# Kernel tuning notes

Measured on AMD Instinct MI355X. Metric: run time of the kernel, lower is better.

The kernel has to match this reference:

```python
import jax, jax.numpy as jnp
import numpy as np

N_NODES = 100000


def gcn_conv(x, edge_index, W, b):
    """PyG-style GCNConv: symmetric-normalized A+I propagation of x @ W, plus bias."""
    n = x.shape[0]
    src, dst = edge_index[0], edge_index[1]
    loops = jnp.arange(n, dtype=src.dtype)
    src = jnp.concatenate([src, loops])  # add self loops
    dst = jnp.concatenate([dst, loops])
    deg = jax.ops.segment_sum(jnp.ones_like(src, dtype=x.dtype), dst, num_segments=n)
    dinv = jnp.where(deg > 0, jax.lax.rsqrt(deg), 0.0)
    norm = dinv[src] * dinv[dst]  # [E+n]
    h = x @ W  # [n, out]
    msg = h[src] * norm[:, None]  # gather + scale
    out = jax.ops.segment_sum(msg, dst, num_segments=n)  # scatter-add
    return out + b


def setup_inputs() -> dict:
    key = jax.random.key(0)
    ks = jax.random.split(key, 5)
    x = jax.random.normal(ks[0], (N_NODES, 4), dtype=jnp.float32)
    edge_index = jax.random.randint(ks[1], (2, 3200000), 0, N_NODES, dtype=jnp.int64)
    W1 = jax.random.normal(ks[2], (4, 64), dtype=jnp.float32) * 0.5
    b1 = jnp.zeros((64,), dtype=jnp.float32)
    W2 = jax.random.normal(ks[3], (64, 32), dtype=jnp.float32) * 0.125
    b2 = jnp.zeros((32,), dtype=jnp.float32)
    return {"x": x, "edge_index": edge_index, "W1": W1, "b1": b1, "W2": W2, "b2": b2}


def reference(x, edge_index, W1, b1, W2, b2):
    h = gcn_conv(x, edge_index, W1, b1)
    h = jax.nn.relu(h)
    # F.dropout with training=False is identity (eval-mode reference)
    h = gcn_conv(h, edge_index, W2, b2)
    return jnp.mean(h, axis=0)  # [32]
```

## Files before the change

### kernel.cpp

```cpp
#include <hip/hip_runtime.h>

#define ST 512
#define EPB 8192
#define HT 1024
#define FT 1024
#define S_LOG 8
#define S 256
#define CAP 8912
#define MAXB 512
#define FXS 8388608.0f
#define FXI 1.1920929e-7f

__device__ __forceinline__ void gAtomAdd(float* p, float v) {
    unsafeAtomicAdd(p, v);
}

__global__ void k_init(int* __restrict__ cur_d, int* __restrict__ cur_s,
                       float* __restrict__ g, int nb) {
    int t = threadIdx.x;
    if (t < nb) { cur_d[t] = t * CAP; cur_s[t] = t * CAP; }
    if (t < 64) g[t] = 0.0f;
}

__global__ void __launch_bounds__(ST) k_sctr2(
        const int4* __restrict__ src4, const int4* __restrict__ dst4, int E,
        int* __restrict__ cur_d, int* __restrict__ cur_s,
        unsigned* __restrict__ rec_d, unsigned* __restrict__ rec_s, int nb) {
    __shared__ unsigned lrec[EPB];
    __shared__ unsigned short lbkt[EPB];
    __shared__ int cnt[MAXB];
    __shared__ int lst[MAXB];
    __shared__ int gb[MAXB];
    __shared__ int wsum[8];
    int t = threadIdx.x;
    int lane = t & 63, wv = t >> 6;
    int E4 = E >> 2;
    int b4 = blockIdx.x * (EPB / 4);
    int m = min(EPB, E - blockIdx.x * EPB);

    int4 dk[4], sk[4];
    bool v[4];
    #pragma unroll
    for (int k = 0; k < 4; ++k) {
        int idx = b4 + k * ST + t;
        v[k] = idx < E4;
        if (v[k]) { dk[k] = dst4[idx]; sk[k] = src4[idx]; }
    }

    for (int ph = 0; ph < 2; ++ph) {
        int* cursor = ph ? cur_s : cur_d;
        unsigned* rec = ph ? rec_s : rec_d;
        cnt[t] = 0;
        __syncthreads();
        int rk[16];
        #pragma unroll
        for (int k = 0; k < 4; ++k) {
            if (v[k]) {
                int4 K = ph ? sk[k] : dk[k];
                rk[4 * k + 0] = atomicAdd(&cnt[K.x >> S_LOG], 1);
                rk[4 * k + 1] = atomicAdd(&cnt[K.y >> S_LOG], 1);
                rk[4 * k + 2] = atomicAdd(&cnt[K.z >> S_LOG], 1);
                rk[4 * k + 3] = atomicAdd(&cnt[K.w >> S_LOG], 1);
            }
        }
        __syncthreads();
        int c = cnt[t];
        int ic = c;
        #pragma unroll
        for (int o = 1; o < 64; o <<= 1) {
            int u = __shfl_up(ic, o);
            if (lane >= o) ic += u;
        }
        if (lane == 63) wsum[wv] = ic;
        __syncthreads();
        int pre = 0;
        #pragma unroll
        for (int k = 0; k < 7; ++k) pre += (k < wv) ? wsum[k] : 0;
        ic += pre;
        lst[t] = ic - c;
        gb[t] = (c > 0) ? atomicAdd(&cursor[t], c) : 0;
        __syncthreads();
        #pragma unroll
        for (int k = 0; k < 4; ++k) {
            if (v[k]) {
                int4 K = ph ? sk[k] : dk[k];
                int4 P = ph ? dk[k] : sk[k];
                int bb, p;
                bb = K.x >> S_LOG; p = lst[bb] + rk[4 * k + 0];
                lrec[p] = ((unsigned)P.x << S_LOG) | (unsigned)(K.x & (S - 1));
                lbkt[p] = (unsigned short)bb;
                bb = K.y >> S_LOG; p = lst[bb] + rk[4 * k + 1];
                lrec[p] = ((unsigned)P.y << S_LOG) | (unsigned)(K.y & (S - 1));
                lbkt[p] = (unsigned short)bb;
                bb = K.z >> S_LOG; p = lst[bb] + rk[4 * k + 2];
                lrec[p] = ((unsigned)P.z << S_LOG) | (unsigned)(K.z & (S - 1));
                lbkt[p] = (unsigned short)bb;
                bb = K.w >> S_LOG; p = lst[bb] + rk[4 * k + 3];
                lrec[p] = ((unsigned)P.w << S_LOG) | (unsigned)(K.w & (S - 1));
                lbkt[p] = (unsigned short)bb;
            }
        }
        __syncthreads();
        for (int i = t; i < m; i += ST) {
            int bb = lbkt[i];
            rec[gb[bb] + (i - lst[bb])] = lrec[i];
        }
        __syncthreads();
    }
}

__global__ void __launch_bounds__(HT) k_hist(
        const unsigned* __restrict__ rec_d, const int* __restrict__ cur_d,
        const float4* __restrict__ x, float* __restrict__ dinv,
        float4* __restrict__ y, int n) {
    __shared__ int cnt[S];
    int b = blockIdx.x, t = threadIdx.x;
    if (t < S) cnt[t] = 0;
    __syncthreads();
    int lo = b * CAP;
    int m = cur_d[b] - lo;
    int m4 = m >> 2;
    const uint4* rec4 = (const uint4*)(rec_d + lo);
    for (int i = t; i < m4; i += HT) {
        uint4 r = rec4[i];
        atomicAdd(&cnt[r.x & (S - 1)], 1);
        atomicAdd(&cnt[r.y & (S - 1)], 1);
        atomicAdd(&cnt[r.z & (S - 1)], 1);
        atomicAdd(&cnt[r.w & (S - 1)], 1);
    }
    for (int i = (m4 << 2) + t; i < m; i += HT)
        atomicAdd(&cnt[rec_d[lo + i] & (S - 1)], 1);
    __syncthreads();
    int nd = (b << S_LOG) + t;
    if (t < S && nd < n) {
        float dv = rsqrtf((float)cnt[t] + 1.0f);
        dinv[nd] = dv;
        float4 xi = x[nd];
        y[nd] = make_float4(dv * xi.x, dv * xi.y, dv * xi.z, dv * xi.w);
    }
}

__global__ void __launch_bounds__(FT) k_fuse(
        const unsigned* __restrict__ rec_d, const unsigned* __restrict__ rec_s,
        const int* __restrict__ cur_d, const int* __restrict__ cur_s,
        const float4* __restrict__ y, const float* __restrict__ dinv,
        const float* __restrict__ W1, const float* __restrict__ b1,
        float* __restrict__ g, int n) {
    __shared__ unsigned lrec[CAP];
    __shared__ int cnt[S];
    __shared__ int nst[S];
    __shared__ int ia[S];
    __shared__ float4 lp1[S];
    __shared__ float red[FT];
    __shared__ int wsum[4];
    int b = blockIdx.x, t = threadIdx.x;
    int lane = t & 63, wv = t >> 6;
    if (t < S) { cnt[t] = 0; ia[t] = 0; }
    __syncthreads();
    int lo = b * CAP;
    int md = cur_d[b] - lo;
    unsigned rv[9]; int rr[9];
    #pragma unroll
    for (int k = 0; k < 9; ++k) {
        int i = t + k * FT;
        if (i < md) {
            unsigned r = rec_d[lo + i];
            rv[k] = r;
            rr[k] = atomicAdd(&cnt[r & (S - 1)], 1);
        }
    }
    __syncthreads();
    int c = 0, ic = 0;
    if (t < S) {
        c = cnt[t]; ic = c;
        #pragma unroll
        for (int o = 1; o < 64; o <<= 1) {
            int u = __shfl_up(ic, o);
            if (lane >= o) ic += u;
        }
        if (lane == 63) wsum[wv] = ic;
    }
    __syncthreads();
    if (t < S) {
        int pre = 0;
        #pragma unroll
        for (int k = 0; k < 3; ++k) pre += (k < wv) ? wsum[k] : 0;
        ic += pre;
        cnt[t] = ic;
        nst[t] = ic - c;
    }
    __syncthreads();
    #pragma unroll
    for (int k = 0; k < 9; ++k) {
        int i = t + k * FT;
        if (i < md) lrec[nst[rv[k] & (S - 1)] + rr[k]] = rv[k] >> S_LOG;
    }
    int ms = cur_s[b] - lo;
    int ms4 = ms >> 2;
    const uint4* rs4 = (const uint4*)(rec_s + lo);
    for (int i = t; i < ms4; i += FT) {
        uint4 r = rs4[i];
        int d0 = (int)(dinv[r.x >> S_LOG] * FXS + 0.5f);
        int d1 = (int)(dinv[r.y >> S_LOG] * FXS + 0.5f);
        int d2 = (int)(dinv[r.z >> S_LOG] * FXS + 0.5f);
        int d3 = (int)(dinv[r.w >> S_LOG] * FXS + 0.5f);
        atomicAdd(&ia[r.x & (S - 1)], d0);
        atomicAdd(&ia[r.y & (S - 1)], d1);
        atomicAdd(&ia[r.z & (S - 1)], d2);
        atomicAdd(&ia[r.w & (S - 1)], d3);
    }
    for (int i = (ms4 << 2) + t; i < ms; i += FT) {
        unsigned r = rec_s[lo + i];
        atomicAdd(&ia[r & (S - 1)], (int)(dinv[r >> S_LOG] * FXS + 0.5f));
    }
    __syncthreads();
    int node = t >> 2, q = t & 3;
    int nd = (b << S_LOG) + node;
    if (nd < n) {
        int j1 = cnt[node];
        int j = nst[node] + q;
        float a0 = 0.0f, a1 = 0.0f, a2 = 0.0f, a3 = 0.0f;
        for (; j + 12 < j1; j += 16) {
            int s0 = lrec[j], s1 = lrec[j + 4], s2 = lrec[j + 8], s3 = lrec[j + 12];
            float4 y0 = y[s0], y1 = y[s1], y2 = y[s2], y3 = y[s3];
            a0 += y0.x + y1.x + y2.x + y3.x;
            a1 += y0.y + y1.y + y2.y + y3.y;
            a2 += y0.z + y1.z + y2.z + y3.z;
            a3 += y0.w + y1.w + y2.w + y3.w;
        }
        for (; j < j1; j += 4) {
            float4 ys = y[lrec[j]];
            a0 += ys.x; a1 += ys.y; a2 += ys.z; a3 += ys.w;
        }
        a0 += __shfl_down(a0, 2); a1 += __shfl_down(a1, 2);
        a2 += __shfl_down(a2, 2); a3 += __shfl_down(a3, 2);
        a0 += __shfl_down(a0, 1); a1 += __shfl_down(a1, 1);
        a2 += __shfl_down(a2, 1); a3 += __shfl_down(a3, 1);
        if (q == 0) {
            float di = dinv[nd];
            lp1[node] = make_float4(di * a0, di * a1, di * a2, di * a3);
        }
    }
    __syncthreads();
    int cch = t & 63, w = t >> 6;
    float w0 = W1[cch], w1 = W1[64 + cch], w2 = W1[128 + cch], w3 = W1[192 + cch];
    float bb = b1[cch];
    int nb0 = b << S_LOG;
    float facc = 0.0f;
    for (int k = w; k < S; k += 16) {
        int ndk = nb0 + k;
        if (ndk >= n) break;
        float di = dinv[ndk];
        float4 p = lp1[k];
        float4 yi = y[ndk];
        float h0 = fmaf(di, yi.x, p.x);
        float h1 = fmaf(di, yi.y, p.y);
        float h2 = fmaf(di, yi.z, p.z);
        float h3 = fmaf(di, yi.w, p.w);
        float h = fmaf(h0, w0, fmaf(h1, w1, fmaf(h2, w2, fmaf(h3, w3, bb))));
        h = fmaxf(h, 0.0f);
        float ak = (float)ia[k] * FXI;
        float wi = fmaf(di, ak, di * di);
        facc = fmaf(wi, h, facc);
    }
    red[t] = facc;
    __syncthreads();
    if (t < 64) {
        float s = red[t];
        #pragma unroll
        for (int o = 1; o < 16; ++o) s += red[t + 64 * o];
        gAtomAdd(&g[t], s);
    }
}

__global__ void k_final(const float* __restrict__ g, const float* __restrict__ W2,
                        const float* __restrict__ b2, float* __restrict__ out, float inv_n) {
    int j = threadIdx.x;
    if (j < 32) {
        float a = 0.0f;
        #pragma unroll
        for (int c = 0; c < 64; ++c) a = fmaf(g[c], W2[c * 32 + j], a);
        out[j] = fmaf(a, inv_n, b2[j]);
    }
}

extern "C" void kernel_launch(void* const* d_in, const int* in_sizes, int n_in,
                              void* d_out, int out_size, void* d_ws, size_t ws_size,
                              hipStream_t stream) {
    const float* x  = (const float*)d_in[0];
    const int*   ei = (const int*)d_in[1];
    const float* W1 = (const float*)d_in[2];
    const float* b1 = (const float*)d_in[3];
    const float* W2 = (const float*)d_in[4];
    const float* b2 = (const float*)d_in[5];
    float* out = (float*)d_out;

    int n = in_sizes[0] / 4;
    int E = in_sizes[1] / 2;
    const int* src = ei;
    const int* dst = ei + E;
    int NB = (n + S - 1) >> S_LOG;

    char* ws = (char*)d_ws;
    int* cur_d = (int*)ws;
    int* cur_s = cur_d + 512;
    float* g   = (float*)(cur_s + 512);
    size_t ctrl = 1600;
    unsigned* rec_d = (unsigned*)ws + ctrl;
    unsigned* rec_s = rec_d + (size_t)NB * CAP;
    float* y    = (float*)(rec_s + (size_t)NB * CAP);
    float* dinv = y + 4 * (size_t)n;

    int NSB = (E + EPB - 1) / EPB;

    k_init<<<1, 512, 0, stream>>>(cur_d, cur_s, g, NB);
    k_sctr2<<<NSB, ST, 0, stream>>>((const int4*)src, (const int4*)dst, E,
                                    cur_d, cur_s, rec_d, rec_s, NB);
    k_hist<<<NB, HT, 0, stream>>>(rec_d, cur_d, (const float4*)x, dinv,
                                  (float4*)y, n);
    k_fuse<<<NB, FT, 0, stream>>>(rec_d, rec_s, cur_d, cur_s,
                                  (const float4*)y, dinv, W1, b1, g, n);
    k_final<<<1, 64, 0, stream>>>(g, W2, b2, out, 1.0f / (float)n);
}
```

Measured before the change: 146.0 us.

## Fold final projection into fuse kernel, replace init kernel with memset, widen scatter blocks

The separate k_final launch is removed. The last block of k_fuse, found through an atomic ticket counter, now does the 64x32 projection. The init kernel becomes a hipMemsetAsync, with cursors changed to zero-based offsets. The scatter kernel now uses 1024 threads per block with 2 int4 loads per thread instead of 512 threads with 4. Together this cuts launch overhead at the cost of a threadfence/ticket pattern in k_fuse.

```diff
diff --git a/kernel.cpp b/kernel.cpp
--- a/kernel.cpp
+++ b/kernel.cpp
@@ -1,6 +1,6 @@
 #include <hip/hip_runtime.h>
 
-#define ST 512
+#define ST 1024
 #define EPB 8192
 #define HT 1024
 #define FT 1024
@@ -13,13 +13,6 @@
 
 __device__ __forceinline__ void gAtomAdd(float* p, float v) {
     unsafeAtomicAdd(p, v);
-}
-
-__global__ void k_init(int* __restrict__ cur_d, int* __restrict__ cur_s,
-                       float* __restrict__ g, int nb) {
-    int t = threadIdx.x;
-    if (t < nb) { cur_d[t] = t * CAP; cur_s[t] = t * CAP; }
-    if (t < 64) g[t] = 0.0f;
 }
 
 __global__ void __launch_bounds__(ST) k_sctr2(
@@ -38,10 +31,10 @@
     int b4 = blockIdx.x * (EPB / 4);
     int m = min(EPB, E - blockIdx.x * EPB);
 
-    int4 dk[4], sk[4];
-    bool v[4];
+    int4 dk[2], sk[2];
+    bool v[2];
     #pragma unroll
-    for (int k = 0; k < 4; ++k) {
+    for (int k = 0; k < 2; ++k) {
         int idx = b4 + k * ST + t;
         v[k] = idx < E4;
         if (v[k]) { dk[k] = dst4[idx]; sk[k] = src4[idx]; }
@@ -50,11 +43,11 @@
     for (int ph = 0; ph < 2; ++ph) {
         int* cursor = ph ? cur_s : cur_d;
         unsigned* rec = ph ? rec_s : rec_d;
-        cnt[t] = 0;
-        __syncthreads();
-        int rk[16];
-        #pragma unroll
-        for (int k = 0; k < 4; ++k) {
+        if (t < MAXB) cnt[t] = 0;
+        __syncthreads();
+        int rk[8];
+        #pragma unroll
+        for (int k = 0; k < 2; ++k) {
             if (v[k]) {
                 int4 K = ph ? sk[k] : dk[k];
                 rk[4 * k + 0] = atomicAdd(&cnt[K.x >> S_LOG], 1);
@@ -64,24 +57,28 @@
             }
         }
         __syncthreads();
-        int c = cnt[t];
-        int ic = c;
-        #pragma unroll
-        for (int o = 1; o < 64; o <<= 1) {
-            int u = __shfl_up(ic, o);
-            if (lane >= o) ic += u;
-        }
-        if (lane == 63) wsum[wv] = ic;
-        __syncthreads();
-        int pre = 0;
-        #pragma unroll
-        for (int k = 0; k < 7; ++k) pre += (k < wv) ? wsum[k] : 0;
-        ic += pre;
-        lst[t] = ic - c;
-        gb[t] = (c > 0) ? atomicAdd(&cursor[t], c) : 0;
-        __syncthreads();
-        #pragma unroll
-        for (int k = 0; k < 4; ++k) {
+        int c = 0, ic = 0;
+        if (t < MAXB) {
+            c = cnt[t]; ic = c;
+            #pragma unroll
+            for (int o = 1; o < 64; o <<= 1) {
+                int u = __shfl_up(ic, o);
+                if (lane >= o) ic += u;
+            }
+            if (lane == 63) wsum[wv] = ic;
+        }
+        __syncthreads();
+        if (t < MAXB) {
+            int pre = 0;
+            #pragma unroll
+            for (int k = 0; k < 7; ++k) pre += (k < wv) ? wsum[k] : 0;
+            ic += pre;
+            lst[t] = ic - c;
+            gb[t] = (c > 0) ? t * CAP + atomicAdd(&cursor[t], c) : 0;
+        }
+        __syncthreads();
+        #pragma unroll
+        for (int k = 0; k < 2; ++k) {
             if (v[k]) {
                 int4 K = ph ? sk[k] : dk[k];
                 int4 P = ph ? dk[k] : sk[k];
@@ -118,7 +115,7 @@
     if (t < S) cnt[t] = 0;
     __syncthreads();
     int lo = b * CAP;
-    int m = cur_d[b] - lo;
+    int m = cur_d[b];
     int m4 = m >> 2;
     const uint4* rec4 = (const uint4*)(rec_d + lo);
     for (int i = t; i < m4; i += HT) {
@@ -145,7 +142,9 @@
         const int* __restrict__ cur_d, const int* __restrict__ cur_s,
         const float4* __restrict__ y, const float* __restrict__ dinv,
         const float* __restrict__ W1, const float* __restrict__ b1,
-        float* __restrict__ g, int n) {
+        const float* __restrict__ W2, const float* __restrict__ b2,
+        float* __restrict__ g, int* __restrict__ done,
+        float* __restrict__ out, float inv_n, int n) {
     __shared__ unsigned lrec[CAP];
     __shared__ int cnt[S];
     __shared__ int nst[S];
@@ -153,12 +152,13 @@
     __shared__ float4 lp1[S];
     __shared__ float red[FT];
     __shared__ int wsum[4];
+    __shared__ int sticket;
     int b = blockIdx.x, t = threadIdx.x;
     int lane = t & 63, wv = t >> 6;
     if (t < S) { cnt[t] = 0; ia[t] = 0; }
     __syncthreads();
     int lo = b * CAP;
-    int md = cur_d[b] - lo;
+    int md = cur_d[b];
     unsigned rv[9]; int rr[9];
     #pragma unroll
     for (int k = 0; k < 9; ++k) {
@@ -195,7 +195,7 @@
         int i = t + k * FT;
         if (i < md) lrec[nst[rv[k] & (S - 1)] + rr[k]] = rv[k] >> S_LOG;
     }
-    int ms = cur_s[b] - lo;
+    int ms = cur_s[b];
     int ms4 = ms >> 2;
     const uint4* rs4 = (const uint4*)(rec_s + lo);
     for (int i = t; i < ms4; i += FT) {
@@ -271,16 +271,23 @@
         for (int o = 1; o < 16; ++o) s += red[t + 64 * o];
         gAtomAdd(&g[t], s);
     }
-}
-
-__global__ void k_final(const float* __restrict__ g, const float* __restrict__ W2,
-                        const float* __restrict__ b2, float* __restrict__ out, float inv_n) {
-    int j = threadIdx.x;
-    if (j < 32) {
-        float a = 0.0f;
-        #pragma unroll
-        for (int c = 0; c < 64; ++c) a = fmaf(g[c], W2[c * 32 + j], a);
-        out[j] = fmaf(a, inv_n, b2[j]);
+    __syncthreads();
+    if (t == 0) {
+        __threadfence();
+        sticket = atomicAdd(done, 1);
+    }
+    __syncthreads();
+    if (sticket == (int)gridDim.x - 1) {
+        if (t < 32) {
+            float acc = 0.0f;
+            #pragma unroll
+            for (int cc = 0; cc < 64; ++cc) {
+                float gv = __hip_atomic_load(&g[cc], __ATOMIC_RELAXED,
+                                             __HIP_MEMORY_SCOPE_AGENT);
+                acc = fmaf(gv, W2[cc * 32 + t], acc);
+            }
+            out[t] = fmaf(acc, inv_n, b2[t]);
+        }
     }
 }
 
@@ -305,6 +312,7 @@
     int* cur_d = (int*)ws;
     int* cur_s = cur_d + 512;
     float* g   = (float*)(cur_s + 512);
+    int* done  = (int*)(g + 64);
     size_t ctrl = 1600;
     unsigned* rec_d = (unsigned*)ws + ctrl;
     unsigned* rec_s = rec_d + (size_t)NB * CAP;
@@ -313,12 +321,12 @@
 
     int NSB = (E + EPB - 1) / EPB;
 
-    k_init<<<1, 512, 0, stream>>>(cur_d, cur_s, g, NB);
+    hipMemsetAsync(ws, 0, ctrl * 4, stream);
     k_sctr2<<<NSB, ST, 0, stream>>>((const int4*)src, (const int4*)dst, E,
                                     cur_d, cur_s, rec_d, rec_s, NB);
     k_hist<<<NB, HT, 0, stream>>>(rec_d, cur_d, (const float4*)x, dinv,
                                   (float4*)y, n);
     k_fuse<<<NB, FT, 0, stream>>>(rec_d, rec_s, cur_d, cur_s,
-                                  (const float4*)y, dinv, W1, b1, g, n);
-    k_final<<<1, 64, 0, stream>>>(g, W2, b2, out, 1.0f / (float)n);
-}
+                                  (const float4*)y, dinv, W1, b1, W2, b2,
+                                  g, done, out, 1.0f / (float)n, n);
+}
```

Result: slower. 150.2 us (+2.9%).
